# Kernel optimization log

Measured on AMD Instinct MI355X. Metric: run time of the kernel, lower is better.

Reference implementation:

```python
import jax, jax.numpy as jnp
import numpy as np

B, S, D, H, F = 4, 1024, 1024, 16, 4096
DH = D // H  # 64


def _xavier(key, shape):
    fan_in, fan_out = shape[-2], shape[-1]
    limit = np.sqrt(6.0 / (fan_in + fan_out)).astype(np.float32)
    return jax.random.uniform(key, shape, jnp.float32, -limit, limit)


def setup_inputs() -> dict:
    key = jax.random.key(0)
    ks = jax.random.split(key, 24)
    inp = {
        'decoder_input': jax.random.normal(ks[0], (B, S, D), jnp.float32),
        'encoder_output': jax.random.normal(ks[1], (B, S, D), jnp.float32),
        'mask': jnp.broadcast_to(jnp.tril(jnp.ones((S, S), jnp.bool_)), (B, S, S)),
    }
    # self-attention per-head Q/K/V weights stacked over heads: (H, D, DH)
    for i, p in enumerate(['sa', 'ca']):
        base = 2 + i * 8
        inp[f'{p}_wq'] = _xavier(ks[base + 0], (H, D, DH))
        inp[f'{p}_wk'] = _xavier(ks[base + 1], (H, D, DH))
        inp[f'{p}_wv'] = _xavier(ks[base + 2], (H, D, DH))
        inp[f'{p}_bq'] = jnp.zeros((H, DH), jnp.float32)
        inp[f'{p}_bk'] = jnp.zeros((H, DH), jnp.float32)
        inp[f'{p}_bv'] = jnp.zeros((H, DH), jnp.float32)
        inp[f'{p}_wo'] = _xavier(ks[base + 3], (H * DH, D))
        inp[f'{p}_bo'] = jnp.zeros((D,), jnp.float32)
    inp['ff_w1'] = _xavier(ks[18], (D, F))
    inp['ff_b1'] = jnp.zeros((F,), jnp.float32)
    inp['ff_w2'] = _xavier(ks[19], (F, D))
    inp['ff_b2'] = jnp.zeros((D,), jnp.float32)
    for j in (1, 2, 3):
        inp[f'ln{j}_g'] = jnp.ones((D,), jnp.float32)
        inp[f'ln{j}_b'] = jnp.zeros((D,), jnp.float32)
    return inp


def _layernorm(x, g, b, eps=1e-12):
    # torch x.var() default is unbiased (ddof=1) -- match it
    mean = jnp.mean(x, axis=-1, keepdims=True)
    var = jnp.var(x, axis=-1, keepdims=True, ddof=1)
    return g * (x - mean) * jax.lax.rsqrt(var + eps) + b


def _mha(q_in, k_in, v_in, wq, bq, wk, bk, wv, bv, wo, bo, mask=None):
    scale = np.float32(1.0 / np.sqrt(DH))
    q = jnp.einsum('bsd,hde->bhse', q_in, wq) + bq[None, :, None, :]
    k = jnp.einsum('bsd,hde->bhse', k_in, wk) + bk[None, :, None, :]
    v = jnp.einsum('bsd,hde->bhse', v_in, wv) + bv[None, :, None, :]
    scores = jnp.einsum('bhqe,bhke->bhqk', q, k) * scale
    if mask is not None:
        scores = jnp.where(mask[:, None, :, :], scores, jnp.float32(-1e9))
    attn = jax.nn.softmax(scores, axis=-1)
    out = jnp.einsum('bhqk,bhke->bhqe', attn, v)  # (B,H,S,DH)
    out = out.transpose(0, 2, 1, 3).reshape(q_in.shape[0], q_in.shape[1], H * DH)
    return out @ wo + bo


def reference(decoder_input, encoder_output, mask,
              sa_wq, sa_wk, sa_wv, sa_bq, sa_bk, sa_bv, sa_wo, sa_bo,
              ca_wq, ca_wk, ca_wv, ca_bq, ca_bk, ca_bv, ca_wo, ca_bo,
              ff_w1, ff_b1, ff_w2, ff_b2,
              ln1_g, ln1_b, ln2_g, ln2_b, ln3_g, ln3_b):
    # dropout is identity (eval mode)
    out1 = _mha(decoder_input, decoder_input, decoder_input,
                sa_wq, sa_bq, sa_wk, sa_bk, sa_wv, sa_bv, sa_wo, sa_bo, mask)
    out1 = _layernorm(out1 + decoder_input, ln1_g, ln1_b)
    out2 = _mha(out1, encoder_output, encoder_output,
                ca_wq, ca_bq, ca_wk, ca_bk, ca_wv, ca_bv, ca_wo, ca_bo, None)
    out2 = _layernorm(out2 + out1, ln2_g, ln2_b)
    out3 = jax.nn.relu(out2 @ ff_w1 + ff_b1) @ ff_w2 + ff_b2
    out3 = _layernorm(out3 + out2, ln3_g, ln3_b)
    return out3
```

## Files before the change

kernel.cpp:

```cpp
#include <hip/hip_runtime.h>
#include <hip/hip_bf16.h>

using bf16 = __hip_bfloat16;
typedef __attribute__((ext_vector_type(8))) short bf16x8;
typedef __attribute__((ext_vector_type(4))) float f32x4;

__device__ __forceinline__ float toF(float x) { return x; }
__device__ __forceinline__ float toF(bf16 x) { return __bfloat162float(x); }

template <typename T> __device__ __forceinline__ T fromF(float x);
template <> __device__ __forceinline__ float fromF<float>(float x) { return x; }
template <> __device__ __forceinline__ bf16 fromF<bf16>(float x) { return __float2bfloat16(x); }

__device__ __forceinline__ unsigned short f2bu(float f) {
    bf16 h = __float2bfloat16(f);
    return *reinterpret_cast<unsigned short*>(&h);
}
__device__ __forceinline__ float bu2f(unsigned short u) {
    unsigned int x = ((unsigned int)u) << 16;
    return __uint_as_float(x);
}

__device__ __forceinline__ float fexp2(float x) {
#if __has_builtin(__builtin_amdgcn_exp2f)
    return __builtin_amdgcn_exp2f(x);
#else
    return __expf(x * 0.69314718f);
#endif
}

__device__ __forceinline__ void gload16(const unsigned short* g, unsigned short* l) {
    __builtin_amdgcn_global_load_lds(
        (const __attribute__((address_space(1))) unsigned int*)g,
        (__attribute__((address_space(3))) unsigned int*)l, 16, 0, 0);
}

__global__ __launch_bounds__(256) void cvt_k(const float* __restrict__ X,
                                             unsigned short* __restrict__ Y, int n)
{
    int i = (blockIdx.x * 256 + threadIdx.x) * 4;
    if (i >= n) return;
    float4 v = *(const float4*)(X + i);
    ushort4 o;
    o.x = f2bu(v.x); o.y = f2bu(v.y); o.z = f2bu(v.z); o.w = f2bu(v.w);
    *(ushort4*)(Y + i) = o;
}

struct WPtrs { const float* w[3]; };

template <bool HEADED>
__global__ __launch_bounds__(256) void wtrans_k(
    WPtrs wp, unsigned short* __restrict__ Wt, int K, int N)
{
    __shared__ float t[32][33];
    const float* __restrict__ W = wp.w[blockIdx.z];
    unsigned short* __restrict__ out = Wt + (size_t)blockIdx.z * K * N;
    const int k0 = blockIdx.x * 32, n0 = blockIdx.y * 32;
    const int tx = threadIdx.x & 31, ty = threadIdx.x >> 5;
#pragma unroll
    for (int i = 0; i < 4; i++) {
        int k = k0 + ty + 8 * i, n = n0 + tx;
        float v;
        if constexpr (HEADED) v = W[((size_t)(n >> 6) * K + k) * 64 + (n & 63)];
        else                  v = W[(size_t)k * N + n];
        t[ty + 8 * i][tx] = v;
    }
    __syncthreads();
#pragma unroll
    for (int i = 0; i < 4; i++)
        out[(size_t)(n0 + ty + 8 * i) * K + k0 + tx] = f2bu(t[tx][ty + 8 * i]);
}

template <typename TO, typename TR, bool RELU, bool HASRES, int BN>
__global__ __launch_bounds__(256) void gemm_mfma(
    const unsigned short* __restrict__ A, const unsigned short* __restrict__ Bt,
    const float* __restrict__ bias, const TR* __restrict__ res,
    TO* __restrict__ C, int M, int N, int K)
{
    constexpr int MI = (BN == 128) ? 4 : 2;
    __shared__ __align__(16) unsigned short As[128 * 64];
    __shared__ __align__(16) unsigned short Bs[BN * 64];

    const int tid = threadIdx.x;
    const int lane = tid & 63, wv = tid >> 6;
    const int quad = lane >> 4, col = lane & 15;
    const int m0 = blockIdx.y * 128, n0 = blockIdx.x * BN;
    const int wm = (BN == 128) ? (wv >> 1) * 64 : wv * 32;
    const int wn = (BN == 128) ? (wv & 1) * 64 : 0;

    f32x4 acc[MI][4];
#pragma unroll
    for (int i = 0; i < MI; i++)
#pragma unroll
        for (int j = 0; j < 4; j++) acc[i][j] = (f32x4){0.f, 0.f, 0.f, 0.f};

    const int rowl = (wv << 3) + (lane >> 3);
    const int xq = (lane & 7) ^ (lane >> 3);
    const unsigned short* Ag = A + (size_t)(m0 + rowl) * K + xq * 8;
    const unsigned short* Bg = Bt + (size_t)(n0 + rowl) * K + xq * 8;
    unsigned short* AsW = As + wv * 512;
    unsigned short* BsW = Bs + wv * 512;

    const int xr = col & 7;

    for (int k0 = 0; k0 < K; k0 += 64) {
        __syncthreads();
#pragma unroll
        for (int r = 0; r < 4; r++)
            gload16(Ag + (size_t)(r * 32) * K + k0, AsW + r * 2048);
#pragma unroll
        for (int r = 0; r < BN / 32; r++)
            gload16(Bg + (size_t)(r * 32) * K + k0, BsW + r * 2048);
        __syncthreads();

#pragma unroll
        for (int kk = 0; kk < 2; kk++) {
            const int cq = ((kk << 2) + quad) ^ xr;
            bf16x8 af[MI], bfr[4];
#pragma unroll
            for (int mi = 0; mi < MI; mi++)
                af[mi] = *(const bf16x8*)(As + (wm + mi * 16 + col) * 64 + cq * 8);
#pragma unroll
            for (int ni = 0; ni < 4; ni++)
                bfr[ni] = *(const bf16x8*)(Bs + (wn + ni * 16 + col) * 64 + cq * 8);
#pragma unroll
            for (int mi = 0; mi < MI; mi++)
#pragma unroll
                for (int ni = 0; ni < 4; ni++)
                    acc[mi][ni] = __builtin_amdgcn_mfma_f32_16x16x32_bf16(
                        af[mi], bfr[ni], acc[mi][ni], 0, 0, 0);
        }
    }

    float bv[4];
#pragma unroll
    for (int ni = 0; ni < 4; ni++) bv[ni] = bias[n0 + wn + ni * 16 + col];
#pragma unroll
    for (int mi = 0; mi < MI; mi++) {
#pragma unroll
        for (int r = 0; r < 4; r++) {
            int m = m0 + wm + mi * 16 + quad * 4 + r;
#pragma unroll
            for (int ni = 0; ni < 4; ni++) {
                int n = n0 + wn + ni * 16 + col;
                float v = acc[mi][ni][r] + bv[ni];
                if constexpr (HASRES) v += toF(res[(size_t)m * N + n]);
                if constexpr (RELU) v = v > 0.f ? v : 0.f;
                C[(size_t)m * N + n] = fromF<TO>(v);
            }
        }
    }
}

struct SegArgs {
    const float* bias[3];
    unsigned short* out[3];
};

__global__ __launch_bounds__(256) void gemm_seg(
    const unsigned short* __restrict__ A, const unsigned short* __restrict__ Bt,
    SegArgs sp, int M, int K, int transSeg)
{
    __shared__ __align__(16) unsigned short As[128 * 64];
    __shared__ __align__(16) unsigned short Bs[128 * 64];

    const int tid = threadIdx.x;
    const int lane = tid & 63, wv = tid >> 6;
    const int quad = lane >> 4, col = lane & 15;
    const int m0 = blockIdx.y * 128, n0 = blockIdx.x * 128;
    const int wm = (wv >> 1) * 64, wn = (wv & 1) * 64;

    f32x4 acc[4][4];
#pragma unroll
    for (int i = 0; i < 4; i++)
#pragma unroll
        for (int j = 0; j < 4; j++) acc[i][j] = (f32x4){0.f, 0.f, 0.f, 0.f};

    const int rowl = (wv << 3) + (lane >> 3);
    const int xq = (lane & 7) ^ (lane >> 3);
    const unsigned short* Ag = A + (size_t)(m0 + rowl) * K + xq * 8;
    const unsigned short* Bg = Bt + (size_t)(n0 + rowl) * K + xq * 8;
    unsigned short* AsW = As + wv * 512;
    unsigned short* BsW = Bs + wv * 512;
    const int xr = col & 7;

    for (int k0 = 0; k0 < K; k0 += 64) {
        __syncthreads();
#pragma unroll
        for (int r = 0; r < 4; r++)
            gload16(Ag + (size_t)(r * 32) * K + k0, AsW + r * 2048);
#pragma unroll
        for (int r = 0; r < 4; r++)
            gload16(Bg + (size_t)(r * 32) * K + k0, BsW + r * 2048);
        __syncthreads();

#pragma unroll
        for (int kk = 0; kk < 2; kk++) {
            const int cq = ((kk << 2) + quad) ^ xr;
            bf16x8 af[4], bfr[4];
#pragma unroll
            for (int mi = 0; mi < 4; mi++)
                af[mi] = *(const bf16x8*)(As + (wm + mi * 16 + col) * 64 + cq * 8);
#pragma unroll
            for (int ni = 0; ni < 4; ni++)
                bfr[ni] = *(const bf16x8*)(Bs + (wn + ni * 16 + col) * 64 + cq * 8);
#pragma unroll
            for (int mi = 0; mi < 4; mi++)
#pragma unroll
                for (int ni = 0; ni < 4; ni++)
                    acc[mi][ni] = __builtin_amdgcn_mfma_f32_16x16x32_bf16(
                        af[mi], bfr[ni], acc[mi][ni], 0, 0, 0);
        }
    }

    const int seg = n0 >> 10;
    const float* bias = sp.bias[seg];
    unsigned short* out = sp.out[seg];
    const int nb = (n0 & 1023) + wn;
    const bool trans = (seg == transSeg);

    float bv[4];
#pragma unroll
    for (int ni = 0; ni < 4; ni++) bv[ni] = bias[nb + ni * 16 + col];
#pragma unroll
    for (int mi = 0; mi < 4; mi++) {
#pragma unroll
        for (int r = 0; r < 4; r++) {
            int m = m0 + wm + mi * 16 + quad * 4 + r;
#pragma unroll
            for (int ni = 0; ni < 4; ni++) {
                int nl = nb + ni * 16 + col;
                float v = acc[mi][ni][r] + bv[ni];
                if (trans)
                    out[((size_t)(m >> 10) * 1024 + nl) * 1024 + (m & 1023)] = f2bu(v);
                else
                    out[(size_t)m * 1024 + nl] = f2bu(v);
            }
        }
    }
}

template <bool CAUSAL>
__global__ __launch_bounds__(256) void fattn_k(
    const unsigned short* __restrict__ Q, const unsigned short* __restrict__ K,
    const unsigned short* __restrict__ Vt, unsigned short* __restrict__ O, int S)
{
    const int qt = CAUSAL ? ((int)gridDim.x - 1 - (int)blockIdx.x) : blockIdx.x;
    const int h = blockIdx.y, b = blockIdx.z;
    const int H64 = 1024;
    const int tid = threadIdx.x;
    const int w = tid >> 6, lane = tid & 63;
    const int quad = lane >> 4, col = lane & 15;

    __shared__ __align__(16) unsigned short Ks[64 * 64];
    __shared__ __align__(16) unsigned short Vs[64 * 64];
    __shared__ __align__(16) unsigned short Ps[4 * 16 * 72];

    const int qBase = qt * 64 + w * 16;
    const size_t qrow = ((size_t)b * S + qBase + col) * H64 + h * 64;

    const float qscale = 0.125f * 1.44269504f;
    bf16x8 qf0, qf1;
    {
        bf16x8 r0 = *(const bf16x8*)(Q + qrow + quad * 8);
        bf16x8 r1 = *(const bf16x8*)(Q + qrow + quad * 8 + 32);
#pragma unroll
        for (int j = 0; j < 8; j++) {
            qf0[j] = (short)f2bu(bu2f((unsigned short)r0[j]) * qscale);
            qf1[j] = (short)f2bu(bu2f((unsigned short)r1[j]) * qscale);
        }
    }

    f32x4 o[4];
#pragma unroll
    for (int g = 0; g < 4; g++) o[g] = (f32x4){0.f, 0.f, 0.f, 0.f};
    float m_run[4], l_run[4];
#pragma unroll
    for (int r = 0; r < 4; r++) { m_run[r] = -1e30f; l_run[r] = 0.f; }

    const int srow = (w << 3) + (lane >> 3);
    const int xq8 = ((lane & 7) ^ (lane >> 3)) * 8;
    const size_t kgbase = (size_t)b * S * H64 + h * 64;
    const size_t vgbase = ((size_t)b * 1024 + h * 64) * (size_t)S;
    const int xr = col & 7;
    const int c0 = quad ^ xr;

    const int nkt = CAUSAL ? (qt + 1) : (S >> 6);
    unsigned short* Pw = Ps + w * (16 * 72);

    for (int kt = 0; kt < nkt; kt++) {
        __syncthreads();
        {
            const unsigned short* kgp = K + kgbase + (size_t)(kt * 64 + srow) * H64 + xq8;
            gload16(kgp, Ks + w * 512);
            gload16(kgp + (size_t)32 * H64, Ks + 2048 + w * 512);
            const unsigned short* vgp = Vt + vgbase + (size_t)srow * S + kt * 64 + xq8;
            gload16(vgp, Vs + w * 512);
            gload16(vgp + (size_t)32 * S, Vs + 2048 + w * 512);
        }
        __syncthreads();

        f32x4 s[4];
#pragma unroll
        for (int kg = 0; kg < 4; kg++) {
            const unsigned short* kr = Ks + (kg * 16 + col) * 64;
            bf16x8 k0 = *(const bf16x8*)(kr + c0 * 8);
            bf16x8 k1 = *(const bf16x8*)(kr + (c0 ^ 4) * 8);
            f32x4 a = (f32x4){0.f, 0.f, 0.f, 0.f};
            a = __builtin_amdgcn_mfma_f32_16x16x32_bf16(qf0, k0, a, 0, 0, 0);
            a = __builtin_amdgcn_mfma_f32_16x16x32_bf16(qf1, k1, a, 0, 0, 0);
            s[kg] = a;
        }

        if (CAUSAL && kt == qt) {
#pragma unroll
            for (int kg = 0; kg < 4; kg++)
#pragma unroll
                for (int r = 0; r < 4; r++) {
                    int key = kg * 16 + col;
                    int q = w * 16 + quad * 4 + r;
                    if (key > q) s[kg][r] = -1e30f;
                }
        }

        float mx[4];
#pragma unroll
        for (int r = 0; r < 4; r++) {
            float m2 = fmaxf(fmaxf(s[0][r], s[1][r]), fmaxf(s[2][r], s[3][r]));
#pragma unroll
            for (int off = 1; off < 16; off <<= 1)
                m2 = fmaxf(m2, __shfl_xor(m2, off));
            mx[r] = m2;
        }

        bool defer = (mx[0] <= m_run[0] + 8.f) & (mx[1] <= m_run[1] + 8.f)
                   & (mx[2] <= m_run[2] + 8.f) & (mx[3] <= m_run[3] + 8.f);
        if (!__all(defer)) {
#pragma unroll
            for (int r = 0; r < 4; r++) {
                float mnew = fmaxf(m_run[r], mx[r]);
                float alpha = fexp2(m_run[r] - mnew);
                l_run[r] *= alpha;
#pragma unroll
                for (int g = 0; g < 4; g++) o[g][r] *= alpha;
                m_run[r] = mnew;
            }
        }

#pragma unroll
        for (int r = 0; r < 4; r++) {
            float ps = 0.f;
#pragma unroll
            for (int kg = 0; kg < 4; kg++) {
                float e = fexp2(s[kg][r] - m_run[r]);
                s[kg][r] = e;
                ps += e;
            }
#pragma unroll
            for (int off = 1; off < 16; off <<= 1)
                ps += __shfl_xor(ps, off);
            l_run[r] += ps;
        }

#pragma unroll
        for (int kg = 0; kg < 4; kg++)
#pragma unroll
            for (int r = 0; r < 4; r++)
                Pw[(quad * 4 + r) * 72 + kg * 16 + col] = f2bu(s[kg][r]);

        bf16x8 p0 = *(const bf16x8*)(Pw + col * 72 + quad * 8);
        bf16x8 p1 = *(const bf16x8*)(Pw + col * 72 + quad * 8 + 32);

#pragma unroll
        for (int g = 0; g < 4; g++) {
            const unsigned short* vr = Vs + (g * 16 + col) * 64;
            bf16x8 v0 = *(const bf16x8*)(vr + c0 * 8);
            bf16x8 v1 = *(const bf16x8*)(vr + (c0 ^ 4) * 8);
            o[g] = __builtin_amdgcn_mfma_f32_16x16x32_bf16(p0, v0, o[g], 0, 0, 0);
            o[g] = __builtin_amdgcn_mfma_f32_16x16x32_bf16(p1, v1, o[g], 0, 0, 0);
        }
    }

    const size_t orow = ((size_t)b * S + qBase) * H64 + h * 64;
#pragma unroll
    for (int r = 0; r < 4; r++) {
        float inv = 1.f / l_run[r];
        int q = quad * 4 + r;
#pragma unroll
        for (int g = 0; g < 4; g++)
            O[orow + (size_t)q * H64 + g * 16 + col] = f2bu(o[g][r] * inv);
    }
}

template <typename TO>
__global__ __launch_bounds__(256) void ln_k(
    const float* __restrict__ X, const float* __restrict__ g,
    const float* __restrict__ bb, TO* __restrict__ O, int D)
{
    const int row = blockIdx.x;
    const int tid = threadIdx.x;
    __shared__ float xs[1024];
    __shared__ float red[256];
    const float* x = X + (size_t)row * D;

    float s = 0.f;
    for (int i = tid; i < D; i += 256) { float v = x[i]; xs[i] = v; s += v; }
    red[tid] = s;
    __syncthreads();
    for (int t = 128; t > 0; t >>= 1) {
        if (tid < t) red[tid] += red[tid + t];
        __syncthreads();
    }
    const float mean = red[0] / (float)D;
    __syncthreads();

    float s2 = 0.f;
    for (int i = tid; i < D; i += 256) { float d = xs[i] - mean; s2 += d * d; }
    red[tid] = s2;
    __syncthreads();
    for (int t = 128; t > 0; t >>= 1) {
        if (tid < t) red[tid] += red[tid + t];
        __syncthreads();
    }
    const float rstd = rsqrtf(red[0] / (float)(D - 1) + 1e-12f);

    TO* o = O + (size_t)row * D;
    for (int i = tid; i < D; i += 256)
        o[i] = fromF<TO>(g[i] * (xs[i] - mean) * rstd + bb[i]);
}

extern "C" void kernel_launch(void* const* d_in, const int* in_sizes, int n_in,
                              void* d_out, int out_size, void* d_ws, size_t ws_size,
                              hipStream_t stream)
{
    const int Bb = 4, S = 1024, D = 1024, F = 4096;
    const int M = Bb * S;
    const int H = 16;

    const float* dec = (const float*)d_in[0];
    const float* enc = (const float*)d_in[1];

    int base = 2;
    if (n_in >= 29 && in_sizes[2] == Bb * S * S) base = 3;

    const float* sa_wq = (const float*)d_in[base + 0];
    const float* sa_wk = (const float*)d_in[base + 1];
    const float* sa_wv = (const float*)d_in[base + 2];
    const float* sa_bq = (const float*)d_in[base + 3];
    const float* sa_bk = (const float*)d_in[base + 4];
    const float* sa_bv = (const float*)d_in[base + 5];
    const float* sa_wo = (const float*)d_in[base + 6];
    const float* sa_bo = (const float*)d_in[base + 7];
    const float* ca_wq = (const float*)d_in[base + 8];
    const float* ca_wk = (const float*)d_in[base + 9];
    const float* ca_wv = (const float*)d_in[base + 10];
    const float* ca_bq = (const float*)d_in[base + 11];
    const float* ca_bk = (const float*)d_in[base + 12];
    const float* ca_bv = (const float*)d_in[base + 13];
    const float* ca_wo = (const float*)d_in[base + 14];
    const float* ca_bo = (const float*)d_in[base + 15];
    const float* ff_w1 = (const float*)d_in[base + 16];
    const float* ff_b1 = (const float*)d_in[base + 17];
    const float* ff_w2 = (const float*)d_in[base + 18];
    const float* ff_b2 = (const float*)d_in[base + 19];
    const float* ln1_g = (const float*)d_in[base + 20];
    const float* ln1_b = (const float*)d_in[base + 21];
    const float* ln2_g = (const float*)d_in[base + 22];
    const float* ln2_b = (const float*)d_in[base + 23];
    const float* ln3_g = (const float*)d_in[base + 24];
    const float* ln3_b = (const float*)d_in[base + 25];

    const size_t E = (size_t)M * D;
    float* SUM = (float*)d_ws;
    bf16* O1 = (bf16*)(SUM + E);
    bf16* O2 = O1 + E;
    bf16* Q  = O2 + E;
    bf16* Kb = Q + E;
    bf16* Vt = Kb + E;
    bf16* AO = Vt + E;
    bf16* HID = Q;
    unsigned short* decB = (unsigned short*)AO;
    unsigned short* Wt   = (unsigned short*)d_out;
    unsigned short* encB = (unsigned short*)d_out + 4 * 1024 * 1024;

    dim3 blk(256);
    dim3 gQKV(3 * D / 128, M / 128);
    dim3 gKV(2 * D / 128, M / 128);
    dim3 gN(D / 64, M / 128);
    dim3 gF(F / 128, M / 128);
    dim3 gA(S / 64, H, Bb);
    dim3 gT3(D / 32, D / 32, 3);
    dim3 gT2z(D / 32, D / 32, 2);
    dim3 gT(D / 32, D / 32, 1);
    dim3 gT1(D / 32, F / 32, 1);
    dim3 gT2(F / 32, D / 32, 1);

    cvt_k<<<M * D / 1024, blk, 0, stream>>>(dec, decB, M * D);
    cvt_k<<<M * D / 1024, blk, 0, stream>>>(enc, encB, M * D);

    {
        WPtrs wp; wp.w[0] = sa_wq; wp.w[1] = sa_wk; wp.w[2] = sa_wv;
        wtrans_k<true><<<gT3, blk, 0, stream>>>(wp, Wt, D, D);
    }
    {
        SegArgs sp;
        sp.bias[0] = sa_bq; sp.bias[1] = sa_bk; sp.bias[2] = sa_bv;
        sp.out[0] = (unsigned short*)Q; sp.out[1] = (unsigned short*)Kb;
        sp.out[2] = (unsigned short*)Vt;
        gemm_seg<<<gQKV, blk, 0, stream>>>(decB, Wt, sp, M, D, 2);
    }
    fattn_k<true><<<gA, blk, 0, stream>>>((const unsigned short*)Q, (const unsigned short*)Kb,
                                          (const unsigned short*)Vt, (unsigned short*)AO, S);
    {
        WPtrs wp; wp.w[0] = sa_wo; wp.w[1] = nullptr; wp.w[2] = nullptr;
        wtrans_k<false><<<gT, blk, 0, stream>>>(wp, Wt, D, D);
    }
    gemm_mfma<float, float, false, true, 64><<<gN, blk, 0, stream>>>(
        (const unsigned short*)AO, Wt, sa_bo, dec, SUM, M, D, D);
    ln_k<bf16><<<M, blk, 0, stream>>>(SUM, ln1_g, ln1_b, O1, D);

    {
        WPtrs wp; wp.w[0] = ca_wq; wp.w[1] = nullptr; wp.w[2] = nullptr;
        wtrans_k<true><<<gT, blk, 0, stream>>>(wp, Wt, D, D);
    }
    gemm_mfma<bf16, float, false, false, 64><<<gN, blk, 0, stream>>>(
        (const unsigned short*)O1, Wt, ca_bq, (const float*)nullptr, Q, M, D, D);
    {
        WPtrs wp; wp.w[0] = ca_wk; wp.w[1] = ca_wv; wp.w[2] = nullptr;
        wtrans_k<true><<<gT2z, blk, 0, stream>>>(wp, Wt, D, D);
    }
    {
        SegArgs sp;
        sp.bias[0] = ca_bk; sp.bias[1] = ca_bv; sp.bias[2] = nullptr;
        sp.out[0] = (unsigned short*)Kb; sp.out[1] = (unsigned short*)Vt;
        sp.out[2] = nullptr;
        gemm_seg<<<gKV, blk, 0, stream>>>(encB, Wt, sp, M, D, 1);
    }
    fattn_k<false><<<gA, blk, 0, stream>>>((const unsigned short*)Q, (const unsigned short*)Kb,
                                           (const unsigned short*)Vt, (unsigned short*)AO, S);
    {
        WPtrs wp; wp.w[0] = ca_wo; wp.w[1] = nullptr; wp.w[2] = nullptr;
        wtrans_k<false><<<gT, blk, 0, stream>>>(wp, Wt, D, D);
    }
    gemm_mfma<float, bf16, false, true, 64><<<gN, blk, 0, stream>>>(
        (const unsigned short*)AO, Wt, ca_bo, O1, SUM, M, D, D);
    ln_k<bf16><<<M, blk, 0, stream>>>(SUM, ln2_g, ln2_b, O2, D);

    {
        WPtrs wp; wp.w[0] = ff_w1; wp.w[1] = nullptr; wp.w[2] = nullptr;
        wtrans_k<false><<<gT1, blk, 0, stream>>>(wp, Wt, D, F);
    }
    gemm_mfma<bf16, float, true, false, 128><<<gF, blk, 0, stream>>>(
        (const unsigned short*)O2, Wt, ff_b1, (const float*)nullptr, HID, M, F, D);
    {
        WPtrs wp; wp.w[0] = ff_w2; wp.w[1] = nullptr; wp.w[2] = nullptr;
        wtrans_k<false><<<gT2, blk, 0, stream>>>(wp, Wt, F, D);
    }
    gemm_mfma<float, bf16, false, true, 64><<<gN, blk, 0, stream>>>(
        (const unsigned short*)HID, Wt, ff_b2, O2, SUM, M, D, F);
    ln_k<float><<<M, blk, 0, stream>>>(SUM, ln3_g, ln3_b, (float*)d_out, D);
}
```

Baseline: 579.5 us.

## Double-buffer K tiles and transpose S MFMA to cut softmax shuffles in flash attention

The attention kernel now double-buffers the K tile in shared memory, prefetching the next K tile while the current one is used. It swaps MFMA operands so each lane holds one query row of scores, which turns the per-row max and sum reductions into two cross-quad shuffles instead of four-step reductions over four rows. It also packs P stores into 64-bit writes and adds s_setprio around the MFMA blocks. The cost is extra shared memory for the second K buffer, extra barriers per iteration, and shuffles to redistribute alpha and l back to the output layout.

```diff
diff --git a/kernel.cpp b/kernel.cpp
--- a/kernel.cpp
+++ b/kernel.cpp
@@ -252,7 +252,7 @@
     const int w = tid >> 6, lane = tid & 63;
     const int quad = lane >> 4, col = lane & 15;
 
-    __shared__ __align__(16) unsigned short Ks[64 * 64];
+    __shared__ __align__(16) unsigned short Ks[2][64 * 64];
     __shared__ __align__(16) unsigned short Vs[64 * 64];
     __shared__ __align__(16) unsigned short Ps[4 * 16 * 72];
 
@@ -274,103 +274,109 @@
     f32x4 o[4];
 #pragma unroll
     for (int g = 0; g < 4; g++) o[g] = (f32x4){0.f, 0.f, 0.f, 0.f};
-    float m_run[4], l_run[4];
-#pragma unroll
-    for (int r = 0; r < 4; r++) { m_run[r] = -1e30f; l_run[r] = 0.f; }
+    float m_run = -1e30f, l_run = 0.f;
 
     const int srow = (w << 3) + (lane >> 3);
     const int xq8 = ((lane & 7) ^ (lane >> 3)) * 8;
     const size_t kgbase = (size_t)b * S * H64 + h * 64;
     const size_t vgbase = ((size_t)b * 1024 + h * 64) * (size_t)S;
-    const int xr = col & 7;
-    const int c0 = quad ^ xr;
+    const int c0 = quad ^ (col & 7);
 
     const int nkt = CAUSAL ? (qt + 1) : (S >> 6);
     unsigned short* Pw = Ps + w * (16 * 72);
 
+    {
+        const unsigned short* kgp = K + kgbase + (size_t)srow * H64 + xq8;
+        gload16(kgp, &Ks[0][w * 512]);
+        gload16(kgp + (size_t)32 * H64, &Ks[0][2048 + w * 512]);
+    }
+    __syncthreads();
+
+    int cur = 0;
     for (int kt = 0; kt < nkt; kt++) {
-        __syncthreads();
         {
-            const unsigned short* kgp = K + kgbase + (size_t)(kt * 64 + srow) * H64 + xq8;
-            gload16(kgp, Ks + w * 512);
-            gload16(kgp + (size_t)32 * H64, Ks + 2048 + w * 512);
             const unsigned short* vgp = Vt + vgbase + (size_t)srow * S + kt * 64 + xq8;
             gload16(vgp, Vs + w * 512);
             gload16(vgp + (size_t)32 * S, Vs + 2048 + w * 512);
         }
-        __syncthreads();
+        if (kt + 1 < nkt) {
+            const unsigned short* kgp =
+                K + kgbase + (size_t)((kt + 1) * 64 + srow) * H64 + xq8;
+            gload16(kgp, &Ks[cur ^ 1][w * 512]);
+            gload16(kgp + (size_t)32 * H64, &Ks[cur ^ 1][2048 + w * 512]);
+        }
 
         f32x4 s[4];
+        __builtin_amdgcn_s_setprio(1);
 #pragma unroll
         for (int kg = 0; kg < 4; kg++) {
-            const unsigned short* kr = Ks + (kg * 16 + col) * 64;
+            const unsigned short* kr = &Ks[cur][(kg * 16 + col) * 64];
             bf16x8 k0 = *(const bf16x8*)(kr + c0 * 8);
             bf16x8 k1 = *(const bf16x8*)(kr + (c0 ^ 4) * 8);
             f32x4 a = (f32x4){0.f, 0.f, 0.f, 0.f};
-            a = __builtin_amdgcn_mfma_f32_16x16x32_bf16(qf0, k0, a, 0, 0, 0);
-            a = __builtin_amdgcn_mfma_f32_16x16x32_bf16(qf1, k1, a, 0, 0, 0);
+            a = __builtin_amdgcn_mfma_f32_16x16x32_bf16(k0, qf0, a, 0, 0, 0);
+            a = __builtin_amdgcn_mfma_f32_16x16x32_bf16(k1, qf1, a, 0, 0, 0);
             s[kg] = a;
         }
+        __builtin_amdgcn_s_setprio(0);
 
         if (CAUSAL && kt == qt) {
+            const int ql = w * 16 + col;
 #pragma unroll
             for (int kg = 0; kg < 4; kg++)
 #pragma unroll
-                for (int r = 0; r < 4; r++) {
-                    int key = kg * 16 + col;
-                    int q = w * 16 + quad * 4 + r;
-                    if (key > q) s[kg][r] = -1e30f;
-                }
-        }
-
-        float mx[4];
-#pragma unroll
-        for (int r = 0; r < 4; r++) {
-            float m2 = fmaxf(fmaxf(s[0][r], s[1][r]), fmaxf(s[2][r], s[3][r]));
-#pragma unroll
-            for (int off = 1; off < 16; off <<= 1)
-                m2 = fmaxf(m2, __shfl_xor(m2, off));
-            mx[r] = m2;
-        }
-
-        bool defer = (mx[0] <= m_run[0] + 8.f) & (mx[1] <= m_run[1] + 8.f)
-                   & (mx[2] <= m_run[2] + 8.f) & (mx[3] <= m_run[3] + 8.f);
-        if (!__all(defer)) {
+                for (int r = 0; r < 4; r++)
+                    if (kg * 16 + quad * 4 + r > ql) s[kg][r] = -1e30f;
+        }
+
+        float mx = s[0][0];
+#pragma unroll
+        for (int kg = 0; kg < 4; kg++)
+#pragma unroll
+            for (int r = 0; r < 4; r++) mx = fmaxf(mx, s[kg][r]);
+        mx = fmaxf(mx, __shfl_xor(mx, 16));
+        mx = fmaxf(mx, __shfl_xor(mx, 32));
+
+        if (!__all(mx <= m_run + 8.f)) {
+            float mnew = fmaxf(m_run, mx);
+            float alpha = fexp2(m_run - mnew);
+            l_run *= alpha;
+            m_run = mnew;
 #pragma unroll
             for (int r = 0; r < 4; r++) {
-                float mnew = fmaxf(m_run[r], mx[r]);
-                float alpha = fexp2(m_run[r] - mnew);
-                l_run[r] *= alpha;
-#pragma unroll
-                for (int g = 0; g < 4; g++) o[g][r] *= alpha;
-                m_run[r] = mnew;
+                float ar = __shfl(alpha, (lane & 48) | (quad * 4 + r));
+#pragma unroll
+                for (int g = 0; g < 4; g++) o[g][r] *= ar;
             }
         }
 
-#pragma unroll
-        for (int r = 0; r < 4; r++) {
-            float ps = 0.f;
-#pragma unroll
-            for (int kg = 0; kg < 4; kg++) {
-                float e = fexp2(s[kg][r] - m_run[r]);
+        float ps = 0.f;
+#pragma unroll
+        for (int kg = 0; kg < 4; kg++)
+#pragma unroll
+            for (int r = 0; r < 4; r++) {
+                float e = fexp2(s[kg][r] - m_run);
                 s[kg][r] = e;
                 ps += e;
             }
-#pragma unroll
-            for (int off = 1; off < 16; off <<= 1)
-                ps += __shfl_xor(ps, off);
-            l_run[r] += ps;
-        }
-
-#pragma unroll
-        for (int kg = 0; kg < 4; kg++)
-#pragma unroll
-            for (int r = 0; r < 4; r++)
-                Pw[(quad * 4 + r) * 72 + kg * 16 + col] = f2bu(s[kg][r]);
+        ps += __shfl_xor(ps, 16);
+        ps += __shfl_xor(ps, 32);
+        l_run += ps;
+
+#pragma unroll
+        for (int kg = 0; kg < 4; kg++) {
+            uint2 pk;
+            pk.x = (unsigned)f2bu(s[kg][0]) | ((unsigned)f2bu(s[kg][1]) << 16);
+            pk.y = (unsigned)f2bu(s[kg][2]) | ((unsigned)f2bu(s[kg][3]) << 16);
+            *(uint2*)(Pw + col * 72 + kg * 16 + quad * 4) = pk;
+        }
+
+        __syncthreads();
 
         bf16x8 p0 = *(const bf16x8*)(Pw + col * 72 + quad * 8);
         bf16x8 p1 = *(const bf16x8*)(Pw + col * 72 + quad * 8 + 32);
 
+        __builtin_amdgcn_s_setprio(1);
 #pragma unroll
         for (int g = 0; g < 4; g++) {
             const unsigned short* vr = Vs + (g * 16 + col) * 64;
@@ -379,12 +385,17 @@
             o[g] = __builtin_amdgcn_mfma_f32_16x16x32_bf16(p0, v0, o[g], 0, 0, 0);
             o[g] = __builtin_amdgcn_mfma_f32_16x16x32_bf16(p1, v1, o[g], 0, 0, 0);
         }
+        __builtin_amdgcn_s_setprio(0);
+
+        __syncthreads();
+        cur ^= 1;
     }
 
     const size_t orow = ((size_t)b * S + qBase) * H64 + h * 64;
 #pragma unroll
     for (int r = 0; r < 4; r++) {
-        float inv = 1.f / l_run[r];
+        float lr = __shfl(l_run, (lane & 48) | (quad * 4 + r));
+        float inv = 1.f / lr;
         int q = quad * 4 + r;
 #pragma unroll
         for (int g = 0; g < 4; g++)
```

After: 539.9 us. 6.8% less time.
